# Optimization experiments

Hardware: AMD Instinct MI355X
Metric: run time of the kernel (lower is better)

Reference implementation:

```python
import jax, jax.numpy as jnp
import numpy as np

HEADS = 16
DIM_HEAD = 64


def rotate_half(t):
    x1, x2 = jnp.split(t, 2, axis=-1)
    return jnp.concatenate((-x2, x1), axis=-1)


def apply_rotary_pos_emb(t, freqs):
    # t: [b, h, n, l], freqs: [n, l]
    seq_len = t.shape[-2]
    freqs = freqs[-seq_len:, :]
    return t * jnp.cos(freqs) + rotate_half(t) * jnp.sin(freqs)


def setup_inputs() -> dict:
    key = jax.random.key(0)
    ks = jax.random.split(key, 6)
    b, n, dim, l = 2, 2048, 1024, 32
    x = jax.random.normal(ks[0], (b, n, dim), dtype=jnp.float32)
    rotary_pos_emb = jax.random.normal(ks[1], (n, l), dtype=jnp.float32)
    s = 0.02
    Wq = jax.random.normal(ks[2], (dim, dim), dtype=jnp.float32) * s
    Wk = jax.random.normal(ks[3], (dim, dim), dtype=jnp.float32) * s
    Wv = jax.random.normal(ks[4], (dim, dim), dtype=jnp.float32) * s
    Wout = jax.random.normal(ks[5], (dim, dim), dtype=jnp.float32) * s
    return {"x": x, "rotary_pos_emb": rotary_pos_emb, "Wq": Wq, "Wk": Wk, "Wv": Wv, "Wout": Wout}


def reference(x, rotary_pos_emb, Wq, Wk, Wv, Wout):
    b, n, _ = x.shape
    h, d = HEADS, DIM_HEAD
    scale = d ** -0.5

    def to_heads(t):
        return t.reshape(b, n, h, d).transpose(0, 2, 1, 3)  # b h n d

    q = to_heads(x @ Wq)
    k = to_heads(x @ Wk)
    v = to_heads(x @ Wv)

    # partial rotary on first l dims of q, k, v (module applies rope to v too)
    l = rotary_pos_emb.shape[-1]

    def rope(t):
        tl, tr = t[..., :l], t[..., l:]
        return jnp.concatenate((apply_rotary_pos_emb(tl, rotary_pos_emb), tr), axis=-1)

    q, k, v = rope(q), rope(k), rope(v)

    dots = jnp.einsum('bhid,bhjd->bhij', q, k) * scale  # [b, h, n, n]
    mask_value = jnp.finfo(dots.dtype).min
    causal = jnp.triu(jnp.ones((n, n), dtype=bool), k=1)  # i < j
    dots = jnp.where(causal[None, None, :, :], mask_value, dots)

    attn = jax.nn.softmax(dots, axis=-1)
    out = jnp.einsum('bhij,bhjd->bhid', attn, v)
    out = out.transpose(0, 2, 1, 3).reshape(b, n, h * d)  # b n (h d)
    return out @ Wout
```

## Files before the change

### kernel.cpp

```cpp
#include <hip/hip_runtime.h>
#include <hip/hip_bf16.h>
#include <stdint.h>

#define BATCH 2
#define SEQ 2048
#define NHEADS 16
#define DIM 1024
#define MTOT 4096
#define LOG2E 1.4426950408889634f
#define QSCALE (0.125f * LOG2E)
#define DEFER_THR 11.54f

typedef __attribute__((ext_vector_type(8))) short s16x8;
typedef __attribute__((ext_vector_type(4))) short s16x4;
typedef __attribute__((ext_vector_type(4))) float f32x4;
typedef unsigned short u16;

__device__ __forceinline__ u16 f2b(float f) {
  union { float f; uint32_t u; } v; v.f = f;
  uint32_t r = v.u + 0x7FFFu + ((v.u >> 16) & 1u);
  return (u16)(r >> 16);
}
__device__ __forceinline__ float b2f(u16 h) {
  union { uint32_t u; float f; } v; v.u = ((uint32_t)h) << 16;
  return v.f;
}
__device__ __forceinline__ uint32_t cvtpk_bf16(float a, float b) {
  uint32_t r;
  asm("v_cvt_pk_bf16_f32 %0, %1, %2" : "=v"(r) : "v"(a), "v"(b));
  return r;
}

__device__ __forceinline__ void gload_lds16(void* lds, const void* g) {
  __builtin_amdgcn_global_load_lds(
      (const __attribute__((address_space(1))) unsigned int*)g,
      (__attribute__((address_space(3))) unsigned int*)lds, 16, 0, 0);
}

__global__ __launch_bounds__(256) void prep_kernel(
    const float* __restrict__ x, const float* __restrict__ Wq,
    const float* __restrict__ Wk, const float* __restrict__ Wv,
    const float* __restrict__ Wo, const float* __restrict__ rot,
    u16* __restrict__ xb, u16* __restrict__ WtAll, float2* __restrict__ cs) {
  __shared__ float tile[32][33];
  int bid = blockIdx.x, t = threadIdx.x;
  if (bid < 4096) {
    int i = (bid * 256 + t) * 4;
    float4 v = *(const float4*)(x + i);
    ushort4 o;
    o.x = f2b(v.x); o.y = f2b(v.y); o.z = f2b(v.z); o.w = f2b(v.w);
    *(ushort4*)(xb + i) = o;
  } else if (bid < 8192) {
    int bb = bid - 4096;
    int z = bb >> 10, xB = bb & 31, yB = (bb >> 5) & 31;
    const float* W = (z == 0) ? Wq : (z == 1) ? Wk : (z == 2) ? Wv : Wo;
    u16* Wt = WtAll + (size_t)z * DIM * DIM;
    int k0 = xB * 32, n0 = yB * 32;
    int tx = t & 31, ty = t >> 5;
#pragma unroll
    for (int i = 0; i < 4; i++) {
      int r = ty + i * 8;
      tile[r][tx] = W[(size_t)(k0 + r) * DIM + n0 + tx];
    }
    __syncthreads();
#pragma unroll
    for (int i = 0; i < 4; i++) {
      int r = ty + i * 8;
      Wt[(size_t)(n0 + r) * DIM + k0 + tx] = f2b(tile[tx][r]);
    }
  } else {
    int i = (bid - 8192) * 256 + t;
    float f = rot[i];
    float s, c;
    __sincosf(f, &s, &c);
    cs[i] = make_float2(c, s);
  }
}

#define NKT 16
__global__ __launch_bounds__(512, 2) void qkv8_kernel(
    const u16* __restrict__ A, const u16* __restrict__ Bt,
    const float2* __restrict__ cs, u16* __restrict__ Qh,
    u16* __restrict__ Kh, u16* __restrict__ Vt) {
  __shared__ u16 lds[2][4][8192];
  const int t = threadIdx.x;
  const int w = t >> 6, l = t & 63;
  const int wr = w >> 2, wc = w & 3;
  const int lr = l & 15, lg = l >> 4;
  const int rowBase = blockIdx.x * 256;
  const int colBase = blockIdx.y * 256;
  const char* Ab = (const char*)(A + (size_t)rowBase * DIM);
  const char* Bb = (const char*)(Bt + (size_t)colBase * DIM);
  const int t16 = t * 16;
  const int swz = ((lr >> 1) & 3) << 4;

  f32x4 acc[8][4];
#pragma unroll
  for (int m = 0; m < 8; m++)
#pragma unroll
    for (int n = 0; n < 4; n++) acc[m][n] = (f32x4){0.f, 0.f, 0.f, 0.f};

  auto stageH = [&](int buf, int kind, int kt) {
    const char* gb = (kind >= 2) ? Bb : Ab;
    int khalf = kind & 1;
    char* ldst = (char*)&lds[buf][kind][0];
#pragma unroll
    for (int i = 0; i < 2; i++) {
      int ob = t16 + i * 8192;
      int row = ob >> 6, cb = ob & 63;
      gload_lds16(ldst + ob,
                  gb + (size_t)row * (DIM * 2) + kt * 128 + khalf * 64 +
                      (cb ^ (((row >> 1) & 3) << 4)));
    }
  };
  auto rdA = [&](int cur, int m, int kk) -> s16x8 {
    int R = wr * 128 + m * 16 + lr;
    return *(const s16x8*)((const char*)&lds[cur][kk][0] + R * 64 + ((lg * 16) ^ swz));
  };
  auto rdB = [&](int cur, int n, int kk) -> s16x8 {
    int R = wc * 64 + n * 16 + lr;
    return *(const s16x8*)((const char*)&lds[cur][2 + kk][0] + R * 64 + ((lg * 16) ^ swz));
  };

  stageH(0, 0, 0); stageH(0, 2, 0); stageH(0, 1, 0); stageH(0, 3, 0);
  stageH(1, 2, 1); stageH(1, 0, 1); stageH(1, 3, 1);

  for (int kt = 0; kt < NKT; ++kt) {
    const int cur = kt & 1, nxt = cur ^ 1;
    if (kt >= NKT - 2) { asm volatile("s_waitcnt vmcnt(0)" ::: "memory"); }
    else               { asm volatile("s_waitcnt vmcnt(6)" ::: "memory"); }
    __builtin_amdgcn_s_barrier();
    __builtin_amdgcn_sched_barrier(0);

    s16x8 af[4], bf[4];
#pragma unroll
    for (int i = 0; i < 4; i++) { af[i] = rdA(cur, i, 0); bf[i] = rdB(cur, i, 0); }
    if (kt + 1 < NKT) stageH(nxt, 1, kt + 1);
    __builtin_amdgcn_s_barrier();
    __builtin_amdgcn_sched_barrier(0);
    __builtin_amdgcn_s_setprio(1);
#pragma unroll
    for (int m = 0; m < 4; m++)
#pragma unroll
      for (int n = 0; n < 4; n++)
        acc[m][n] = __builtin_amdgcn_mfma_f32_16x16x32_bf16(af[m], bf[n], acc[m][n], 0, 0, 0);
    __builtin_amdgcn_s_setprio(0);
    __builtin_amdgcn_s_barrier();
    __builtin_amdgcn_sched_barrier(0);
#pragma unroll
    for (int i = 0; i < 4; i++) af[i] = rdA(cur, 4 + i, 0);
    if (kt + 2 < NKT) stageH(cur, 2, kt + 2);
    __builtin_amdgcn_s_barrier();
    __builtin_amdgcn_sched_barrier(0);
    __builtin_amdgcn_s_setprio(1);
#pragma unroll
    for (int m = 0; m < 4; m++)
#pragma unroll
      for (int n = 0; n < 4; n++)
        acc[4 + m][n] = __builtin_amdgcn_mfma_f32_16x16x32_bf16(af[m], bf[n], acc[4 + m][n], 0, 0, 0);
    __builtin_amdgcn_s_setprio(0);
    __builtin_amdgcn_s_barrier();
    __builtin_amdgcn_sched_barrier(0);
#pragma unroll
    for (int i = 0; i < 4; i++) { af[i] = rdA(cur, i, 1); bf[i] = rdB(cur, i, 1); }
    if (kt + 2 < NKT) stageH(cur, 0, kt + 2);
    __builtin_amdgcn_s_barrier();
    __builtin_amdgcn_sched_barrier(0);
    __builtin_amdgcn_s_setprio(1);
#pragma unroll
    for (int m = 0; m < 4; m++)
#pragma unroll
      for (int n = 0; n < 4; n++)
        acc[m][n] = __builtin_amdgcn_mfma_f32_16x16x32_bf16(af[m], bf[n], acc[m][n], 0, 0, 0);
    __builtin_amdgcn_s_setprio(0);
    __builtin_amdgcn_s_barrier();
    __builtin_amdgcn_sched_barrier(0);
#pragma unroll
    for (int i = 0; i < 4; i++) af[i] = rdA(cur, 4 + i, 1);
    if (kt + 2 < NKT) stageH(cur, 3, kt + 2);
    __builtin_amdgcn_s_barrier();
    __builtin_amdgcn_sched_barrier(0);
    __builtin_amdgcn_s_setprio(1);
#pragma unroll
    for (int m = 0; m < 4; m++)
#pragma unroll
      for (int n = 0; n < 4; n++)
        acc[4 + m][n] = __builtin_amdgcn_mfma_f32_16x16x32_bf16(af[m], bf[n], acc[4 + m][n], 0, 0, 0);
    __builtin_amdgcn_s_setprio(0);
    __builtin_amdgcn_s_barrier();
    __builtin_amdgcn_sched_barrier(0);
  }

  int cg = colBase + wc * 64;
  int z = cg >> 10;
  int h = (cg >> 6) & (NHEADS - 1);
  if (z == 2) {
#pragma unroll
    for (int m = 0; m < 8; m++) {
#pragma unroll
      for (int r = 0; r < 4; r++) {
        int row = rowBase + wr * 128 + m * 16 + lg * 4 + r;
        int nrow = row & (SEQ - 1);
        int b2 = row >> 11;
        const float2* csr = cs + (size_t)nrow * 32;
        float a0 = acc[m][0][r], a1 = acc[m][1][r];
        float2 f0 = csr[lr];
        float2 f1 = csr[16 + lr];
        float o0 = a0 * f0.x - a1 * f0.y;
        float o1 = a1 * f1.x + a0 * f1.y;
        size_t vbase = ((size_t)(b2 * NHEADS + h) * 64) * SEQ + nrow;
        Vt[vbase + (size_t)lr * SEQ]        = f2b(o0);
        Vt[vbase + (size_t)(16 + lr) * SEQ] = f2b(o1);
        Vt[vbase + (size_t)(32 + lr) * SEQ] = f2b(acc[m][2][r]);
        Vt[vbase + (size_t)(48 + lr) * SEQ] = f2b(acc[m][3][r]);
      }
    }
  } else {
    u16* C = (z == 0) ? Qh : Kh;
    float sc = (z == 0) ? QSCALE : 1.0f;
#pragma unroll
    for (int m = 0; m < 8; m++) {
#pragma unroll
      for (int r = 0; r < 4; r++) {
        int row = rowBase + wr * 128 + m * 16 + lg * 4 + r;
        int nrow = row & (SEQ - 1);
        int b2 = row >> 11;
        const float2* csr = cs + (size_t)nrow * 32;
        float a0 = acc[m][0][r], a1 = acc[m][1][r];
        float2 f0 = csr[lr];
        float2 f1 = csr[16 + lr];
        float o0 = (a0 * f0.x - a1 * f0.y) * sc;
        float o1 = (a1 * f1.x + a0 * f1.y) * sc;
        size_t base = ((size_t)(b2 * NHEADS + h) * SEQ + nrow) * 64;
        C[base + lr]      = f2b(o0);
        C[base + 16 + lr] = f2b(o1);
        C[base + 32 + lr] = f2b(acc[m][2][r] * sc);
        C[base + 48 + lr] = f2b(acc[m][3][r] * sc);
      }
    }
  }
}

__global__ __launch_bounds__(256) void gemm_out(
    const u16* __restrict__ A, const u16* __restrict__ Bt,
    float* __restrict__ C) {
  __shared__ u16 Asm[2][64 * 32];
  __shared__ u16 Bsm[2][128 * 32];
  int t = threadIdx.x;
  int w = t >> 6, l = t & 63;
  int wr = w >> 1, wc = w & 1;
  int lr = l & 15, lg = l >> 4;
  int rowBase = blockIdx.x * 64;
  int colBase = blockIdx.y * 128;
  const char* Ab = (const char*)(A + (size_t)rowBase * DIM);
  const char* Bb = (const char*)(Bt + (size_t)colBase * DIM);

  f32x4 acc[2][4];
#pragma unroll
  for (int m = 0; m < 2; m++)
#pragma unroll
    for (int n = 0; n < 4; n++) acc[m][n] = (f32x4){0.f, 0.f, 0.f, 0.f};

  auto stage = [&](int buf, int kt) {
    {
      int ob = t * 16;
      int row = ob >> 6, cb = ob & 63;
      gload_lds16((char*)&Asm[buf][0] + ob,
                  Ab + (size_t)row * (DIM * 2) + kt * 64 + (cb ^ (((row >> 1) & 3) << 4)));
    }
#pragma unroll
    for (int i = 0; i < 2; i++) {
      int ob = t * 16 + i * 4096;
      int row = ob >> 6, cb = ob & 63;
      gload_lds16((char*)&Bsm[buf][0] + ob,
                  Bb + (size_t)row * (DIM * 2) + kt * 64 + (cb ^ (((row >> 1) & 3) << 4)));
    }
  };

  stage(0, 0);
  for (int kt = 0; kt < DIM / 32; ++kt) {
    int cur = kt & 1;
    __syncthreads();
    if (kt + 1 < DIM / 32) stage(cur ^ 1, kt + 1);
    const char* ab = (const char*)&Asm[cur][0];
    const char* bb = (const char*)&Bsm[cur][0];
    s16x8 af[2], bf[4];
#pragma unroll
    for (int m = 0; m < 2; m++) {
      int R = wr * 32 + m * 16 + lr;
      af[m] = *(const s16x8*)(ab + R * 64 + ((lg * 16) ^ (((R >> 1) & 3) << 4)));
    }
#pragma unroll
    for (int n = 0; n < 4; n++) {
      int R = wc * 64 + n * 16 + lr;
      bf[n] = *(const s16x8*)(bb + R * 64 + ((lg * 16) ^ (((R >> 1) & 3) << 4)));
    }
    __builtin_amdgcn_s_setprio(1);
#pragma unroll
    for (int m = 0; m < 2; m++)
#pragma unroll
      for (int n = 0; n < 4; n++)
        acc[m][n] = __builtin_amdgcn_mfma_f32_16x16x32_bf16(af[m], bf[n], acc[m][n], 0, 0, 0);
    __builtin_amdgcn_s_setprio(0);
  }

#pragma unroll
  for (int m = 0; m < 2; m++)
#pragma unroll
    for (int n = 0; n < 4; n++) {
      int row = rowBase + wr * 32 + m * 16 + lg * 4;
      int col = colBase + wc * 64 + n * 16 + lr;
#pragma unroll
      for (int r = 0; r < 4; r++)
        C[(size_t)(row + r) * DIM + col] = acc[m][n][r];
    }
}

__global__ __launch_bounds__(256) void attn_kernel(
    const u16* __restrict__ Qh, const u16* __restrict__ Kh,
    const u16* __restrict__ Vtg, u16* __restrict__ Ob) {
  int id = blockIdx.x;
  int xcd = id & 7, within = id >> 3;
  int bh = xcd * 4 + (within >> 4);
  int pi = within & 15;
  int b = bh >> 4, h = bh & 15;
  __shared__ u16 Ks[2][64 * 64];
  __shared__ u16 Vs[2][64 * 64];
  int t = threadIdx.x, w = t >> 6, l = t & 63;
  int lr = l & 15, lg = l >> 4;

  const char* Kbh = (const char*)(Kh + (size_t)bh * SEQ * 64);
  const char* Vbh = (const char*)Vtg + (size_t)bh * 64 * SEQ * 2;
  const u16* Qbh = Qh + (size_t)bh * SEQ * 64;

  auto stage = [&](int buf, int kt) {
    const char* kg = Kbh + (size_t)kt * 64 * 128;
    const char* vg = Vbh + kt * 128;
#pragma unroll
    for (int i = 0; i < 2; i++) {
      int ob = i * 4096 + t * 16;
      int row = ob >> 7, cb = ob & 127;
      int sw = cb ^ ((row & 7) << 4);
      gload_lds16((char*)&Ks[buf][0] + ob, kg + row * 128 + sw);
      gload_lds16((char*)&Vs[buf][0] + ob, vg + row * 4096 + sw);
    }
  };

#pragma unroll 1
  for (int ph = 0; ph < 2; ++ph) {
    int qt = ph ? (31 - pi) : pi;
    int nkt = qt + 1;
    int qrow = qt * 64 + w * 16 + lr;

    s16x8 qf[2];
#pragma unroll
    for (int kk = 0; kk < 2; kk++)
      qf[kk] = *(const s16x8*)(Qbh + (size_t)qrow * 64 + kk * 32 + lg * 8);

    f32x4 o[4];
#pragma unroll
    for (int dt = 0; dt < 4; dt++) o[dt] = (f32x4){0.f, 0.f, 0.f, 0.f};
    float mrun = -3.0e38f, lsum = 0.f;

    __syncthreads();
    stage(0, 0);
    for (int kt = 0; kt < nkt; ++kt) {
      int cur = kt & 1;
      __syncthreads();
      if (kt + 1 < nkt) stage(cur ^ 1, kt + 1);
      const char* kb = (const char*)&Ks[cur][0];
      const char* vb = (const char*)&Vs[cur][0];

      f32x4 s[4];
#pragma unroll
      for (int n = 0; n < 4; n++) s[n] = (f32x4){0.f, 0.f, 0.f, 0.f};
      __builtin_amdgcn_s_setprio(1);
#pragma unroll
      for (int n = 0; n < 4; n++)
#pragma unroll
        for (int kk = 0; kk < 2; kk++) {
          int R = n * 16 + lr;
          s16x8 kf = *(const s16x8*)(kb + R * 128 + ((kk * 64 + lg * 16) ^ ((R & 7) << 4)));
          s[n] = __builtin_amdgcn_mfma_f32_16x16x32_bf16(kf, qf[kk], s[n], 0, 0, 0);
        }
      __builtin_amdgcn_s_setprio(0);

      if (kt == nkt - 1) {
#pragma unroll
        for (int n = 0; n < 4; n++) {
          int kbase = kt * 64 + n * 16 + lg * 4;
#pragma unroll
          for (int r = 0; r < 4; r++)
            if (kbase + r > qrow) s[n][r] = -3.0e38f;
        }
      }

      float mloc;
      {
        float m0 = fmaxf(fmaxf(s[0][0], s[0][1]), fmaxf(s[0][2], s[0][3]));
        float m1 = fmaxf(fmaxf(s[1][0], s[1][1]), fmaxf(s[1][2], s[1][3]));
        float m2 = fmaxf(fmaxf(s[2][0], s[2][1]), fmaxf(s[2][2], s[2][3]));
        float m3 = fmaxf(fmaxf(s[3][0], s[3][1]), fmaxf(s[3][2], s[3][3]));
        mloc = fmaxf(fmaxf(m0, m1), fmaxf(m2, m3));
      }
      mloc = fmaxf(mloc, __shfl_xor(mloc, 16, 64));
      mloc = fmaxf(mloc, __shfl_xor(mloc, 32, 64));
      if (!__all(mloc - mrun <= DEFER_THR)) {
        float mn = fmaxf(mrun, mloc);
        float alpha = exp2f(mrun - mn);
        mrun = mn; lsum *= alpha;
#pragma unroll
        for (int dt = 0; dt < 4; dt++)
#pragma unroll
          for (int r = 0; r < 4; r++) o[dt][r] *= alpha;
      }
      float p[4][4];
#pragma unroll
      for (int n = 0; n < 4; n++)
#pragma unroll
        for (int r = 0; r < 4; r++) p[n][r] = exp2f(s[n][r] - mrun);
      lsum += ((p[0][0] + p[0][1]) + (p[0][2] + p[0][3])) +
              ((p[1][0] + p[1][1]) + (p[1][2] + p[1][3])) +
              ((p[2][0] + p[2][1]) + (p[2][2] + p[2][3])) +
              ((p[3][0] + p[3][1]) + (p[3][2] + p[3][3]));

      s16x4 pb[4];
#pragma unroll
      for (int n = 0; n < 4; n++) {
        union { uint32_t u[2]; s16x4 v; } pu;
        pu.u[0] = cvtpk_bf16(p[n][0], p[n][1]);
        pu.u[1] = cvtpk_bf16(p[n][2], p[n][3]);
        pb[n] = pu.v;
      }

      __builtin_amdgcn_s_setprio(1);
#pragma unroll
      for (int dt = 0; dt < 4; dt++) {
        int R = dt * 16 + lr;
#pragma unroll
        for (int n = 0; n < 4; n++) {
          s16x4 vf = *(const s16x4*)(vb + R * 128 + ((n * 32 + lg * 8) ^ ((R & 7) << 4)));
          o[dt] = __builtin_amdgcn_mfma_f32_16x16x16bf16_1k(vf, pb[n], o[dt], 0, 0, 0);
        }
      }
      __builtin_amdgcn_s_setprio(0);
    }

    float sum = lsum;
    sum += __shfl_xor(sum, 16, 64);
    sum += __shfl_xor(sum, 32, 64);
    float inv = 1.0f / sum;
    u16* orow = Ob + ((size_t)b * SEQ + qrow) * DIM + h * 64 + lg * 4;
#pragma unroll
    for (int dt = 0; dt < 4; dt++) {
      ushort4 ov;
      ov.x = f2b(o[dt][0] * inv); ov.y = f2b(o[dt][1] * inv);
      ov.z = f2b(o[dt][2] * inv); ov.w = f2b(o[dt][3] * inv);
      *(ushort4*)(orow + dt * 16) = ov;
    }
  }
}

extern "C" void kernel_launch(void* const* d_in, const int* in_sizes, int n_in,
                              void* d_out, int out_size, void* d_ws, size_t ws_size,
                              hipStream_t stream) {
  (void)in_sizes; (void)n_in; (void)out_size; (void)ws_size;
  const float* x = (const float*)d_in[0];
  const float* rot = (const float*)d_in[1];
  const float* Wq = (const float*)d_in[2];
  const float* Wk = (const float*)d_in[3];
  const float* Wv = (const float*)d_in[4];
  const float* Wo = (const float*)d_in[5];

  char* ws = (char*)d_ws;
  u16* xb    = (u16*)(ws);
  u16* WtAll = (u16*)(ws + (8ll << 20));
  u16* Qh    = (u16*)(ws + (16ll << 20));
  u16* Kh    = (u16*)(ws + (24ll << 20));
  u16* Vt    = (u16*)(ws + (32ll << 20));
  u16* Ob    = (u16*)(ws + (40ll << 20));
  float2* cs = (float2*)(ws + (48ll << 20));

  prep_kernel<<<8448, 256, 0, stream>>>(x, Wq, Wk, Wv, Wo, rot, xb, WtAll, cs);
  qkv8_kernel<<<dim3(16, 12), 512, 0, stream>>>(xb, WtAll, cs, Qh, Kh, Vt);
  attn_kernel<<<512, 256, 0, stream>>>(Qh, Kh, Vt, Ob);
  gemm_out<<<dim3(64, 8), 256, 0, stream>>>(Ob, WtAll + 3ll * DIM * DIM, (float*)d_out);
}
```

Baseline: 200.2 us.

## Retile QKV GEMM to 256x192 blocks and change V LDS swizzle in attention

The QKV projection GEMM moves from 256x256 tiles on a 16x12 grid to 256x192 tiles on a 16x16 grid, so 256 blocks cover the 256 CUs. It also restructures LDS staging into separate A half-K buffers and a full-K B buffer, and uses a generic per-column epilogue with RoPE and head scatter. Separately, the attention kernel stages V with 4-byte global-to-LDS loads under a finer swizzle to reduce LDS bank conflicts on the transposed V reads. The tradeoffs are more global load instructions for V, and a per-element epilogue with branches and scattered 2-byte stores.

```diff
diff --git a/kernel.cpp b/kernel.cpp
--- a/kernel.cpp
+++ b/kernel.cpp
@@ -35,6 +35,11 @@
   __builtin_amdgcn_global_load_lds(
       (const __attribute__((address_space(1))) unsigned int*)g,
       (__attribute__((address_space(3))) unsigned int*)lds, 16, 0, 0);
+}
+__device__ __forceinline__ void gload_lds4(void* lds, const void* g) {
+  __builtin_amdgcn_global_load_lds(
+      (const __attribute__((address_space(1))) unsigned int*)g,
+      (__attribute__((address_space(3))) unsigned int*)lds, 4, 0, 0);
 }
 
 __global__ __launch_bounds__(256) void prep_kernel(
@@ -78,164 +83,162 @@
 }
 
 #define NKT 16
-__global__ __launch_bounds__(512, 2) void qkv8_kernel(
+__global__ __launch_bounds__(512) void qkv192_kernel(
     const u16* __restrict__ A, const u16* __restrict__ Bt,
     const float2* __restrict__ cs, u16* __restrict__ Qh,
     u16* __restrict__ Kh, u16* __restrict__ Vt) {
-  __shared__ u16 lds[2][4][8192];
+  __shared__ u16 Albuf[2][2][8192];
+  __shared__ u16 Bbuf[2][12288];
   const int t = threadIdx.x;
   const int w = t >> 6, l = t & 63;
-  const int wr = w >> 2, wc = w & 3;
+  const int wr = w >> 1, wc = w & 1;
   const int lr = l & 15, lg = l >> 4;
   const int rowBase = blockIdx.x * 256;
-  const int colBase = blockIdx.y * 256;
+  const int colBase = blockIdx.y * 192;
   const char* Ab = (const char*)(A + (size_t)rowBase * DIM);
   const char* Bb = (const char*)(Bt + (size_t)colBase * DIM);
   const int t16 = t * 16;
-  const int swz = ((lr >> 1) & 3) << 4;
-
-  f32x4 acc[8][4];
-#pragma unroll
-  for (int m = 0; m < 8; m++)
-#pragma unroll
-    for (int n = 0; n < 4; n++) acc[m][n] = (f32x4){0.f, 0.f, 0.f, 0.f};
-
-  auto stageH = [&](int buf, int kind, int kt) {
-    const char* gb = (kind >= 2) ? Bb : Ab;
-    int khalf = kind & 1;
-    char* ldst = (char*)&lds[buf][kind][0];
+
+  f32x4 acc[4][6];
+#pragma unroll
+  for (int m = 0; m < 4; m++)
+#pragma unroll
+    for (int n = 0; n < 6; n++) acc[m][n] = (f32x4){0.f, 0.f, 0.f, 0.f};
+
+  auto stageA = [&](int buf, int kh, int kt) {
+    char* ldst = (char*)&Albuf[buf][kh][0];
 #pragma unroll
     for (int i = 0; i < 2; i++) {
       int ob = t16 + i * 8192;
       int row = ob >> 6, cb = ob & 63;
       gload_lds16(ldst + ob,
-                  gb + (size_t)row * (DIM * 2) + kt * 128 + khalf * 64 +
+                  Ab + (size_t)row * 2048 + kt * 128 + kh * 64 +
                       (cb ^ (((row >> 1) & 3) << 4)));
     }
   };
-  auto rdA = [&](int cur, int m, int kk) -> s16x8 {
-    int R = wr * 128 + m * 16 + lr;
-    return *(const s16x8*)((const char*)&lds[cur][kk][0] + R * 64 + ((lg * 16) ^ swz));
+  auto stageB = [&](int buf, int kt) {
+    char* ldst = (char*)&Bbuf[buf][0];
+#pragma unroll
+    for (int i = 0; i < 3; i++) {
+      int ob = t16 + i * 8192;
+      int row = ob >> 7, cb = ob & 127;
+      gload_lds16(ldst + ob,
+                  Bb + (size_t)row * 2048 + kt * 128 + (cb ^ ((row & 7) << 4)));
+    }
+  };
+  auto rdA = [&](int cur, int kh, int m) -> s16x8 {
+    int R = wr * 64 + m * 16 + lr;
+    return *(const s16x8*)((const char*)&Albuf[cur][kh][0] + R * 64 +
+                           ((lg * 16) ^ (((R >> 1) & 3) << 4)));
   };
   auto rdB = [&](int cur, int n, int kk) -> s16x8 {
-    int R = wc * 64 + n * 16 + lr;
-    return *(const s16x8*)((const char*)&lds[cur][2 + kk][0] + R * 64 + ((lg * 16) ^ swz));
-  };
-
-  stageH(0, 0, 0); stageH(0, 2, 0); stageH(0, 1, 0); stageH(0, 3, 0);
-  stageH(1, 2, 1); stageH(1, 0, 1); stageH(1, 3, 1);
+    int R = wc * 96 + n * 16 + lr;
+    return *(const s16x8*)((const char*)&Bbuf[cur][0] + R * 128 +
+                           ((kk * 64 + lg * 16) ^ ((R & 7) << 4)));
+  };
+
+  stageA(0, 0, 0); stageA(0, 1, 0); stageB(0, 0); stageA(1, 0, 1);
 
   for (int kt = 0; kt < NKT; ++kt) {
     const int cur = kt & 1, nxt = cur ^ 1;
-    if (kt >= NKT - 2) { asm volatile("s_waitcnt vmcnt(0)" ::: "memory"); }
-    else               { asm volatile("s_waitcnt vmcnt(6)" ::: "memory"); }
-    __builtin_amdgcn_s_barrier();
-    __builtin_amdgcn_sched_barrier(0);
-
-    s16x8 af[4], bf[4];
-#pragma unroll
-    for (int i = 0; i < 4; i++) { af[i] = rdA(cur, i, 0); bf[i] = rdB(cur, i, 0); }
-    if (kt + 1 < NKT) stageH(nxt, 1, kt + 1);
+    if (kt == NKT - 1) { asm volatile("s_waitcnt vmcnt(0)" ::: "memory"); }
+    else               { asm volatile("s_waitcnt vmcnt(2)" ::: "memory"); }
+    __builtin_amdgcn_s_barrier();
+    __builtin_amdgcn_sched_barrier(0);
+
+    s16x8 af[4], bf[3];
+#pragma unroll
+    for (int i = 0; i < 4; i++) af[i] = rdA(cur, 0, i);
+#pragma unroll
+    for (int j = 0; j < 3; j++) bf[j] = rdB(cur, j, 0);
+    if (kt + 1 < NKT) { stageA(nxt, 1, kt + 1); stageB(nxt, kt + 1); }
     __builtin_amdgcn_s_barrier();
     __builtin_amdgcn_sched_barrier(0);
     __builtin_amdgcn_s_setprio(1);
 #pragma unroll
     for (int m = 0; m < 4; m++)
 #pragma unroll
-      for (int n = 0; n < 4; n++)
+      for (int n = 0; n < 3; n++)
         acc[m][n] = __builtin_amdgcn_mfma_f32_16x16x32_bf16(af[m], bf[n], acc[m][n], 0, 0, 0);
     __builtin_amdgcn_s_setprio(0);
     __builtin_amdgcn_s_barrier();
     __builtin_amdgcn_sched_barrier(0);
 #pragma unroll
-    for (int i = 0; i < 4; i++) af[i] = rdA(cur, 4 + i, 0);
-    if (kt + 2 < NKT) stageH(cur, 2, kt + 2);
+    for (int j = 0; j < 3; j++) bf[j] = rdB(cur, 3 + j, 0);
+    if (kt + 2 < NKT) stageA(cur, 0, kt + 2);
     __builtin_amdgcn_s_barrier();
     __builtin_amdgcn_sched_barrier(0);
     __builtin_amdgcn_s_setprio(1);
 #pragma unroll
     for (int m = 0; m < 4; m++)
 #pragma unroll
-      for (int n = 0; n < 4; n++)
-        acc[4 + m][n] = __builtin_amdgcn_mfma_f32_16x16x32_bf16(af[m], bf[n], acc[4 + m][n], 0, 0, 0);
+      for (int n = 0; n < 3; n++)
+        acc[m][3 + n] = __builtin_amdgcn_mfma_f32_16x16x32_bf16(af[m], bf[n], acc[m][3 + n], 0, 0, 0);
     __builtin_amdgcn_s_setprio(0);
     __builtin_amdgcn_s_barrier();
     __builtin_amdgcn_sched_barrier(0);
 #pragma unroll
-    for (int i = 0; i < 4; i++) { af[i] = rdA(cur, i, 1); bf[i] = rdB(cur, i, 1); }
-    if (kt + 2 < NKT) stageH(cur, 0, kt + 2);
+    for (int i = 0; i < 4; i++) af[i] = rdA(cur, 1, i);
+#pragma unroll
+    for (int j = 0; j < 3; j++) bf[j] = rdB(cur, j, 1);
     __builtin_amdgcn_s_barrier();
     __builtin_amdgcn_sched_barrier(0);
     __builtin_amdgcn_s_setprio(1);
 #pragma unroll
     for (int m = 0; m < 4; m++)
 #pragma unroll
-      for (int n = 0; n < 4; n++)
+      for (int n = 0; n < 3; n++)
         acc[m][n] = __builtin_amdgcn_mfma_f32_16x16x32_bf16(af[m], bf[n], acc[m][n], 0, 0, 0);
     __builtin_amdgcn_s_setprio(0);
     __builtin_amdgcn_s_barrier();
     __builtin_amdgcn_sched_barrier(0);
 #pragma unroll
-    for (int i = 0; i < 4; i++) af[i] = rdA(cur, 4 + i, 1);
-    if (kt + 2 < NKT) stageH(cur, 3, kt + 2);
+    for (int j = 0; j < 3; j++) bf[j] = rdB(cur, 3 + j, 1);
     __builtin_amdgcn_s_barrier();
     __builtin_amdgcn_sched_barrier(0);
     __builtin_amdgcn_s_setprio(1);
 #pragma unroll
     for (int m = 0; m < 4; m++)
 #pragma unroll
-      for (int n = 0; n < 4; n++)
-        acc[4 + m][n] = __builtin_amdgcn_mfma_f32_16x16x32_bf16(af[m], bf[n], acc[4 + m][n], 0, 0, 0);
+      for (int n = 0; n < 3; n++)
+        acc[m][3 + n] = __builtin_amdgcn_mfma_f32_16x16x32_bf16(af[m], bf[n], acc[m][3 + n], 0, 0, 0);
     __builtin_amdgcn_s_setprio(0);
     __builtin_amdgcn_s_barrier();
     __builtin_amdgcn_sched_barrier(0);
   }
 
-  int cg = colBase + wc * 64;
-  int z = cg >> 10;
-  int h = (cg >> 6) & (NHEADS - 1);
-  if (z == 2) {
-#pragma unroll
-    for (int m = 0; m < 8; m++) {
-#pragma unroll
-      for (int r = 0; r < 4; r++) {
-        int row = rowBase + wr * 128 + m * 16 + lg * 4 + r;
-        int nrow = row & (SEQ - 1);
-        int b2 = row >> 11;
-        const float2* csr = cs + (size_t)nrow * 32;
-        float a0 = acc[m][0][r], a1 = acc[m][1][r];
-        float2 f0 = csr[lr];
-        float2 f1 = csr[16 + lr];
-        float o0 = a0 * f0.x - a1 * f0.y;
-        float o1 = a1 * f1.x + a0 * f1.y;
-        size_t vbase = ((size_t)(b2 * NHEADS + h) * 64) * SEQ + nrow;
-        Vt[vbase + (size_t)lr * SEQ]        = f2b(o0);
-        Vt[vbase + (size_t)(16 + lr) * SEQ] = f2b(o1);
-        Vt[vbase + (size_t)(32 + lr) * SEQ] = f2b(acc[m][2][r]);
-        Vt[vbase + (size_t)(48 + lr) * SEQ] = f2b(acc[m][3][r]);
-      }
-    }
-  } else {
-    u16* C = (z == 0) ? Qh : Kh;
-    float sc = (z == 0) ? QSCALE : 1.0f;
-#pragma unroll
-    for (int m = 0; m < 8; m++) {
-#pragma unroll
-      for (int r = 0; r < 4; r++) {
-        int row = rowBase + wr * 128 + m * 16 + lg * 4 + r;
-        int nrow = row & (SEQ - 1);
-        int b2 = row >> 11;
-        const float2* csr = cs + (size_t)nrow * 32;
-        float a0 = acc[m][0][r], a1 = acc[m][1][r];
-        float2 f0 = csr[lr];
-        float2 f1 = csr[16 + lr];
-        float o0 = (a0 * f0.x - a1 * f0.y) * sc;
-        float o1 = (a1 * f1.x + a0 * f1.y) * sc;
-        size_t base = ((size_t)(b2 * NHEADS + h) * SEQ + nrow) * 64;
-        C[base + lr]      = f2b(o0);
-        C[base + 16 + lr] = f2b(o1);
-        C[base + 32 + lr] = f2b(acc[m][2][r] * sc);
-        C[base + 48 + lr] = f2b(acc[m][3][r] * sc);
+#pragma unroll
+  for (int m = 0; m < 4; m++) {
+#pragma unroll
+    for (int r = 0; r < 4; r++) {
+      int row = rowBase + wr * 64 + m * 16 + lg * 4 + r;
+      int nrow = row & (SEQ - 1);
+      int b2 = row >> 11;
+      const float2* csr = cs + (size_t)nrow * 32;
+#pragma unroll
+      for (int n = 0; n < 6; n++) {
+        int cg = colBase + wc * 96 + n * 16 + lr;
+        int z = cg >> 10;
+        int h = (cg >> 6) & (NHEADS - 1);
+        int hd = cg & 63;
+        float a = acc[m][n][r];
+        float val;
+        if (hd < 16) {
+          float2 f = csr[hd];
+          val = a * f.x - acc[m][n ^ 1][r] * f.y;
+        } else if (hd < 32) {
+          float2 f = csr[hd];
+          val = a * f.x + acc[m][n ^ 1][r] * f.y;
+        } else {
+          val = a;
+        }
+        if (z == 0) {
+          Qh[((size_t)(b2 * NHEADS + h) * SEQ + nrow) * 64 + hd] = f2b(val * QSCALE);
+        } else if (z == 1) {
+          Kh[((size_t)(b2 * NHEADS + h) * SEQ + nrow) * 64 + hd] = f2b(val);
+        } else {
+          Vt[((size_t)(b2 * NHEADS + h) * 64 + hd) * SEQ + nrow] = f2b(val);
+        }
       }
     }
   }
@@ -340,9 +343,13 @@
     for (int i = 0; i < 2; i++) {
       int ob = i * 4096 + t * 16;
       int row = ob >> 7, cb = ob & 127;
-      int sw = cb ^ ((row & 7) << 4);
-      gload_lds16((char*)&Ks[buf][0] + ob, kg + row * 128 + sw);
-      gload_lds16((char*)&Vs[buf][0] + ob, vg + row * 4096 + sw);
+      gload_lds16((char*)&Ks[buf][0] + ob, kg + row * 128 + (cb ^ ((row & 7) << 4)));
+    }
+#pragma unroll
+    for (int i = 0; i < 8; i++) {
+      int ob = i * 1024 + t * 4;
+      int row = ob >> 7, cb = ob & 127;
+      gload_lds4((char*)&Vs[buf][0] + ob, vg + (size_t)row * 4096 + (cb ^ ((row & 15) << 3)));
     }
   };
 
@@ -439,7 +446,7 @@
         int R = dt * 16 + lr;
 #pragma unroll
         for (int n = 0; n < 4; n++) {
-          s16x4 vf = *(const s16x4*)(vb + R * 128 + ((n * 32 + lg * 8) ^ ((R & 7) << 4)));
+          s16x4 vf = *(const s16x4*)(vb + R * 128 + ((n * 32 + lg * 8) ^ ((R & 15) << 3)));
           o[dt] = __builtin_amdgcn_mfma_f32_16x16x16bf16_1k(vf, pb[n], o[dt], 0, 0, 0);
         }
       }
@@ -482,7 +489,7 @@
   float2* cs = (float2*)(ws + (48ll << 20));
 
   prep_kernel<<<8448, 256, 0, stream>>>(x, Wq, Wk, Wv, Wo, rot, xb, WtAll, cs);
-  qkv8_kernel<<<dim3(16, 12), 512, 0, stream>>>(xb, WtAll, cs, Qh, Kh, Vt);
+  qkv192_kernel<<<dim3(16, 16), 512, 0, stream>>>(xb, WtAll, cs, Qh, Kh, Vt);
   attn_kernel<<<512, 256, 0, stream>>>(Qh, Kh, Vt, Ob);
   gemm_out<<<dim3(64, 8), 256, 0, stream>>>(Ob, WtAll + 3ll * DIM * DIM, (float*)d_out);
 }
```

Measured after the change: 220.7 us. 1.1x slower.
